# Kernel tuning notes

Measured on AMD Instinct MI355X. Metric: run time of the kernel, lower is better.

## Reference

```python
import jax, jax.numpy as jnp
import numpy as np

D = 1024
H = 16
HEAD_DIM = D // H

def setup_inputs() -> dict:
    key = jax.random.key(0)
    ks = jax.random.split(key, 5)
    B, T = 2, 2048
    scale = 0.02
    x = jax.random.normal(ks[0], (B, T, D), dtype=jnp.float32)
    W_kqv = jax.random.normal(ks[1], (D, 3 * D), dtype=jnp.float32) * scale
    b_kqv = jnp.zeros((3 * D,), dtype=jnp.float32)
    W_proj = jax.random.normal(ks[2], (D, D), dtype=jnp.float32) * scale
    b_proj = jnp.zeros((D,), dtype=jnp.float32)
    return {"x": x, "W_kqv": W_kqv, "b_kqv": b_kqv, "W_proj": W_proj, "b_proj": b_proj}

def reference(x, W_kqv, b_kqv, W_proj, b_proj):
    B, T, d = x.shape
    qkv = x @ W_kqv + b_kqv  # [B,T,3d]
    q, k, v = jnp.split(qkv, 3, axis=-1)
    # [B, h, T, head_dim]
    def heads(t):
        return t.reshape(B, T, H, HEAD_DIM).transpose(0, 2, 1, 3)
    q, k, v = heads(q), heads(k), heads(v)
    scores = jnp.einsum("bhqd,bhkd->bhqk", q, k) / jnp.sqrt(jnp.float32(HEAD_DIM))
    causal = jnp.tril(jnp.ones((T, T), dtype=bool))  # True = keep
    scores = jnp.where(causal[None, None], scores, -jnp.inf)
    attn = jax.nn.softmax(scores, axis=-1)
    out = jnp.einsum("bhqk,bhkd->bhqd", attn, v)
    out = out.transpose(0, 2, 1, 3).reshape(B, T, d)
    return out @ W_proj + b_proj
```

## Files before the change

kernel.cpp:

```cpp
#include <hip/hip_runtime.h>
#include <hip/hip_bf16.h>
#include <cstdint>

typedef __bf16 bf16_t;
typedef __bf16 bf16x8 __attribute__((ext_vector_type(8)));
typedef __bf16 bf16x4 __attribute__((ext_vector_type(4)));
typedef float  f32x4  __attribute__((ext_vector_type(4)));

static constexpr int Bb = 2;
static constexpr int Tt = 2048;
static constexpr int Dd = 1024;
static constexpr int Hh = 16;
static constexpr int HD = 64;

#define QSCALE 0.18033688011112042f

__device__ __forceinline__ void async_copy16(const bf16_t* gsrc, bf16_t* ldst) {
    __builtin_amdgcn_global_load_lds(
        (const __attribute__((address_space(1))) unsigned int*)gsrc,
        (__attribute__((address_space(3))) unsigned int*)ldst, 16, 0, 0);
}

__global__ __launch_bounds__(256) void prep_kernel(
    const float* __restrict__ x, bf16_t* __restrict__ x_bf,
    const float* __restrict__ Wk, bf16_t* __restrict__ wkqvt,
    const float* __restrict__ Wp, bf16_t* __restrict__ wprojt) {
    __shared__ bf16_t tile[64][72];
    int bid = blockIdx.x;
    int t = threadIdx.x;
    if (bid < 2048) {
        int i = (bid * 256 + t) * 8;
        float4 v0 = *(const float4*)(x + i);
        float4 v1 = *(const float4*)(x + i + 4);
        bf16x8 o;
        o[0] = (bf16_t)v0.x; o[1] = (bf16_t)v0.y; o[2] = (bf16_t)v0.z; o[3] = (bf16_t)v0.w;
        o[4] = (bf16_t)v1.x; o[5] = (bf16_t)v1.y; o[6] = (bf16_t)v1.z; o[7] = (bf16_t)v1.w;
        *(bf16x8*)(x_bf + i) = o;
        return;
    }
    const float* in; bf16_t* out; int R, C, tr, tc;
    if (bid < 2816) {
        int id = bid - 2048;
        R = Dd; C = 3 * Dd;
        tc = (id % 48) * 64; tr = (id / 48) * 64;
        in = Wk; out = wkqvt;
    } else {
        int id = bid - 2816;
        R = Dd; C = Dd;
        tc = (id & 15) * 64; tr = (id >> 4) * 64;
        in = Wp; out = wprojt;
    }
    int r = t >> 4;
    int c4 = (t & 15) * 4;
#pragma unroll
    for (int rr = 0; rr < 4; ++rr) {
        int row = r + rr * 16;
        float4 v = *(const float4*)(in + (size_t)(tr + row) * C + tc + c4);
        tile[c4 + 0][row] = (bf16_t)v.x;
        tile[c4 + 1][row] = (bf16_t)v.y;
        tile[c4 + 2][row] = (bf16_t)v.z;
        tile[c4 + 3][row] = (bf16_t)v.w;
    }
    __syncthreads();
#pragma unroll
    for (int rr = 0; rr < 4; ++rr) {
        int oc = r + rr * 16;
        bf16x4 o;
        o[0] = tile[oc][c4 + 0];
        o[1] = tile[oc][c4 + 1];
        o[2] = tile[oc][c4 + 2];
        o[3] = tile[oc][c4 + 3];
        *(bf16x4*)(out + (size_t)(tc + oc) * R + tr + c4) = o;
    }
}

template <int MODE, int NT>
__global__ __launch_bounds__(256) void gemm_bt(
    const bf16_t* __restrict__ A, const bf16_t* __restrict__ Bt,
    const float* __restrict__ bias, float* __restrict__ Cout,
    bf16_t* __restrict__ qb_, bf16_t* __restrict__ kb_, bf16_t* __restrict__ vb_,
    int M, int N, int K) {
    constexpr int NFRAG = NT / 32;
    __shared__ bf16_t As[128 * 64];
    __shared__ bf16_t Bs[NT * 64];
    int t = threadIdx.x;
    int wave = t >> 6, lane = t & 63;
    int l15 = lane & 15, quad = lane >> 4;
    int wm = wave & 1, wn = wave >> 1;
    int m0 = blockIdx.y * 128, n0 = blockIdx.x * NT;

    f32x4 acc[4][NFRAG];
#pragma unroll
    for (int mi = 0; mi < 4; ++mi)
#pragma unroll
        for (int ni = 0; ni < NFRAG; ++ni) acc[mi][ni] = (f32x4){0.f, 0.f, 0.f, 0.f};

    int kx = l15 & 7;

    for (int kk = 0; kk < K; kk += 64) {
        __syncthreads();
#pragma unroll
        for (int j = 0; j < 4; ++j) {
            int cid = j * 256 + t;
            int row = cid >> 3, sub = (cid & 7) ^ (row & 7);
            async_copy16(A + (size_t)(m0 + row) * K + kk + sub * 8, &As[cid * 8]);
        }
#pragma unroll
        for (int j = 0; j < NT / 32; ++j) {
            int cid = j * 256 + t;
            int row = cid >> 3, sub = (cid & 7) ^ (row & 7);
            async_copy16(Bt + (size_t)(n0 + row) * K + kk + sub * 8, &Bs[cid * 8]);
        }
        __syncthreads();
#pragma unroll
        for (int kb = 0; kb < 2; ++kb) {
            bf16x8 af[4], bf[NFRAG];
#pragma unroll
            for (int mi = 0; mi < 4; ++mi) {
                int r = wm * 64 + mi * 16 + l15;
                af[mi] = *(const bf16x8*)(&As[r * 64 + ((kb * 4 + quad) ^ kx) * 8]);
            }
#pragma unroll
            for (int ni = 0; ni < NFRAG; ++ni) {
                int r = wn * (NT / 2) + ni * 16 + l15;
                bf[ni] = *(const bf16x8*)(&Bs[r * 64 + ((kb * 4 + quad) ^ kx) * 8]);
            }
#pragma unroll
            for (int mi = 0; mi < 4; ++mi)
#pragma unroll
                for (int ni = 0; ni < NFRAG; ++ni)
                    acc[mi][ni] = __builtin_amdgcn_mfma_f32_16x16x32_bf16(af[mi], bf[ni], acc[mi][ni], 0, 0, 0);
        }
    }

    if (MODE == 1 && (n0 >> 10) == 2) {
#pragma unroll
        for (int ni = 0; ni < NFRAG; ++ni) {
            int col = n0 + wn * (NT / 2) + ni * 16 + l15;
            float bv = bias[col];
            int hh = (col >> 6) & 15, dd = col & 63;
#pragma unroll
            for (int mi = 0; mi < 4; ++mi) {
                int row = m0 + wm * 64 + mi * 16 + quad * 4;
                int bb = row >> 11, tt = row & (Tt - 1);
                bf16x4 pv;
#pragma unroll
                for (int r = 0; r < 4; ++r) pv[r] = (bf16_t)(acc[mi][ni][r] + bv);
                *(bf16x4*)(vb_ + ((size_t)(bb * Hh + hh) * HD + dd) * Tt + tt) = pv;
            }
        }
        return;
    }

#pragma unroll
    for (int ni = 0; ni < NFRAG; ++ni) {
        int col = n0 + wn * (NT / 2) + ni * 16 + l15;
        float bv = bias[col];
#pragma unroll
        for (int mi = 0; mi < 4; ++mi) {
#pragma unroll
            for (int r = 0; r < 4; ++r) {
                int row = m0 + wm * 64 + mi * 16 + quad * 4 + r;
                float v = acc[mi][ni][r] + bv;
                if (MODE == 0) {
                    Cout[(size_t)row * N + col] = v;
                } else {
                    int sec = col >> 10;
                    int hh = (col >> 6) & 15, dd = col & 63;
                    int bb = row >> 11, tt = row & (Tt - 1);
                    size_t idx = (((size_t)(bb * Hh + hh)) * Tt + tt) * HD + dd;
                    if (sec == 0) qb_[idx] = (bf16_t)(v * QSCALE);
                    else          kb_[idx] = (bf16_t)v;
                }
            }
        }
    }
}

__global__ __launch_bounds__(256, 4) void attn_kernel(
    const bf16_t* __restrict__ qb, const bf16_t* __restrict__ kb,
    const bf16_t* __restrict__ vb, bf16_t* __restrict__ ab) {
    __shared__ bf16_t Ks[64][72];
    __shared__ bf16_t Vs[64][72];
    __shared__ bf16_t Ps[4][16][72];
    int t = threadIdx.x;
    int wave = t >> 6, lane = t & 63;
    int l15 = lane & 15, quad = lane >> 4;
    int bh = blockIdx.x;
    int qt = 31 - (int)blockIdx.y;
    int b = bh >> 4, h = bh & 15;
    int qbase = qt * 64 + wave * 16;
    int q = qbase + l15;
    const bf16_t* qptr = qb + (size_t)bh * Tt * HD;
    const bf16_t* kptr = kb + (size_t)bh * Tt * HD;
    const bf16_t* vptr = vb + (size_t)bh * HD * Tt;

    bf16x8 qf[2];
    qf[0] = *(const bf16x8*)(qptr + (size_t)q * HD + quad * 8);
    qf[1] = *(const bf16x8*)(qptr + (size_t)q * HD + 32 + quad * 8);

    f32x4 o[4];
#pragma unroll
    for (int g = 0; g < 4; ++g) o[g] = (f32x4){0.f, 0.f, 0.f, 0.f};
    float mrow = -1e30f, lrow = 0.f;

    int srow = t >> 2;
    int scol = (t & 3) * 16;
    int qmax_w = qbase + 15;

    int nkt = qt + 1;
    for (int it = 0; it < nkt; ++it) {
        int kt0 = it * 64;
        __syncthreads();
        const bf16_t* kg = kptr + (size_t)(kt0 + srow) * HD + scol;
        *(bf16x8*)(&Ks[srow][scol])     = *(const bf16x8*)(kg);
        *(bf16x8*)(&Ks[srow][scol + 8]) = *(const bf16x8*)(kg + 8);
        const bf16_t* vg = vptr + (size_t)srow * Tt + kt0 + scol;
        *(bf16x8*)(&Vs[srow][scol])     = *(const bf16x8*)(vg);
        *(bf16x8*)(&Vs[srow][scol + 8]) = *(const bf16x8*)(vg + 8);
        __syncthreads();
        if (kt0 > qmax_w) continue;

        f32x4 s[4];
#pragma unroll
        for (int g = 0; g < 4; ++g) {
            s[g] = (f32x4){0.f, 0.f, 0.f, 0.f};
            bf16x8 kf0 = *(const bf16x8*)(&Ks[g * 16 + l15][quad * 8]);
            bf16x8 kf1 = *(const bf16x8*)(&Ks[g * 16 + l15][32 + quad * 8]);
            s[g] = __builtin_amdgcn_mfma_f32_16x16x32_bf16(kf0, qf[0], s[g], 0, 0, 0);
            s[g] = __builtin_amdgcn_mfma_f32_16x16x32_bf16(kf1, qf[1], s[g], 0, 0, 0);
        }

        if (kt0 + 63 > qbase) {
#pragma unroll
            for (int g = 0; g < 4; ++g)
#pragma unroll
                for (int r = 0; r < 4; ++r) {
                    int k_abs = kt0 + g * 16 + quad * 4 + r;
                    s[g][r] = (k_abs > q) ? -1e30f : s[g][r];
                }
        }

        float mloc = -1e30f;
#pragma unroll
        for (int g = 0; g < 4; ++g)
            mloc = fmaxf(mloc, fmaxf(fmaxf(s[g][0], s[g][1]), fmaxf(s[g][2], s[g][3])));
        mloc = fmaxf(mloc, __shfl_xor(mloc, 16));
        mloc = fmaxf(mloc, __shfl_xor(mloc, 32));
        float mnew = fmaxf(mrow, mloc);
        float alpha = exp2f(mrow - mnew);
        mrow = mnew;

        float rs = 0.f;
#pragma unroll
        for (int g = 0; g < 4; ++g) {
            float p0 = exp2f(s[g][0] - mnew);
            float p1 = exp2f(s[g][1] - mnew);
            float p2 = exp2f(s[g][2] - mnew);
            float p3 = exp2f(s[g][3] - mnew);
            rs += (p0 + p1) + (p2 + p3);
            bf16x4 pk;
            pk[0] = (bf16_t)p0; pk[1] = (bf16_t)p1; pk[2] = (bf16_t)p2; pk[3] = (bf16_t)p3;
            *(bf16x4*)(&Ps[wave][l15][g * 16 + quad * 4]) = pk;
        }
        rs += __shfl_xor(rs, 16);
        rs += __shfl_xor(rs, 32);
        lrow = lrow * alpha + rs;

#pragma unroll
        for (int g = 0; g < 4; ++g)
#pragma unroll
            for (int r = 0; r < 4; ++r) o[g][r] *= alpha;

#pragma unroll
        for (int kc = 0; kc < 2; ++kc) {
            bf16x8 pf = *(const bf16x8*)(&Ps[wave][l15][kc * 32 + quad * 8]);
#pragma unroll
            for (int g = 0; g < 4; ++g) {
                bf16x8 vf = *(const bf16x8*)(&Vs[g * 16 + l15][kc * 32 + quad * 8]);
                o[g] = __builtin_amdgcn_mfma_f32_16x16x32_bf16(vf, pf, o[g], 0, 0, 0);
            }
        }
    }

    float inv = 1.0f / lrow;
    size_t obase = ((size_t)b * Tt + q) * Dd + h * 64;
#pragma unroll
    for (int g = 0; g < 4; ++g) {
        bf16x4 ov;
#pragma unroll
        for (int r = 0; r < 4; ++r) ov[r] = (bf16_t)(o[g][r] * inv);
        *(bf16x4*)(ab + obase + g * 16 + quad * 4) = ov;
    }
}

extern "C" void kernel_launch(void* const* d_in, const int* in_sizes, int n_in,
                              void* d_out, int out_size, void* d_ws, size_t ws_size,
                              hipStream_t stream) {
    const float* x      = (const float*)d_in[0];
    const float* W_kqv  = (const float*)d_in[1];
    const float* b_kqv  = (const float*)d_in[2];
    const float* W_proj = (const float*)d_in[3];
    const float* b_proj = (const float*)d_in[4];
    float* out = (float*)d_out;
    char* ws = (char*)d_ws;
    const size_t MB = 1ull << 20;
    bf16_t* x_bf   = (bf16_t*)(ws + 0 * MB);
    bf16_t* wkqvt  = (bf16_t*)(ws + 8 * MB);
    bf16_t* wprojt = (bf16_t*)(ws + 14 * MB);
    bf16_t* qb     = (bf16_t*)(ws + 16 * MB);
    bf16_t* kb     = (bf16_t*)(ws + 24 * MB);
    bf16_t* vb     = (bf16_t*)(ws + 32 * MB);
    bf16_t* ab     = (bf16_t*)(ws + 40 * MB);

    prep_kernel<<<3072, 256, 0, stream>>>(x, x_bf, W_kqv, wkqvt, W_proj, wprojt);
    gemm_bt<1, 128><<<dim3(3 * Dd / 128, Bb * Tt / 128), 256, 0, stream>>>(
        x_bf, wkqvt, b_kqv, nullptr, qb, kb, vb, Bb * Tt, 3 * Dd, Dd);
    attn_kernel<<<dim3(Bb * Hh, 32), 256, 0, stream>>>(qb, kb, vb, ab);
    gemm_bt<0, 64><<<dim3(Dd / 64, Bb * Tt / 128), 256, 0, stream>>>(
        ab, wprojt, b_proj, out, nullptr, nullptr, nullptr, Bb * Tt, Dd, Dd);
}
```

Measured before the change: 194.2 us.

## Prefetch next K/V tile into registers and vectorize GEMM epilogue stores

The attention kernel now loads the next K/V tile from global memory into registers while the current tile is being computed, so global latency overlaps with MFMA work. The early-skip check for fully masked tiles is removed. Separately, the GEMM swaps the MFMA operand order so each lane holds four consecutive output columns. This allows float4 bias loads and vectorized f32x4/bf16x4 stores for the output, Q and K epilogues, at the cost of scattered scalar stores for the transposed V layout. Register pressure in the attention kernel rises from holding the prefetched tile.

```diff
diff --git a/kernel.cpp b/kernel.cpp
--- a/kernel.cpp
+++ b/kernel.cpp
@@ -129,50 +129,58 @@
             for (int mi = 0; mi < 4; ++mi)
 #pragma unroll
                 for (int ni = 0; ni < NFRAG; ++ni)
-                    acc[mi][ni] = __builtin_amdgcn_mfma_f32_16x16x32_bf16(af[mi], bf[ni], acc[mi][ni], 0, 0, 0);
-        }
-    }
-
-    if (MODE == 1 && (n0 >> 10) == 2) {
+                    acc[mi][ni] = __builtin_amdgcn_mfma_f32_16x16x32_bf16(bf[ni], af[mi], acc[mi][ni], 0, 0, 0);
+        }
+    }
+
+    int sec = n0 >> 10;
+    if (MODE == 1 && sec == 2) {
 #pragma unroll
         for (int ni = 0; ni < NFRAG; ++ni) {
-            int col = n0 + wn * (NT / 2) + ni * 16 + l15;
-            float bv = bias[col];
-            int hh = (col >> 6) & 15, dd = col & 63;
+            int n = n0 + wn * (NT / 2) + ni * 16 + quad * 4;
+            int hh = (n >> 6) & 15, dd0 = n & 63;
+            f32x4 bv4 = *(const f32x4*)(bias + n);
 #pragma unroll
             for (int mi = 0; mi < 4; ++mi) {
-                int row = m0 + wm * 64 + mi * 16 + quad * 4;
+                int row = m0 + wm * 64 + mi * 16 + l15;
+                int bb = row >> 11, tt = row & (Tt - 1);
+#pragma unroll
+                for (int r = 0; r < 4; ++r)
+                    vb_[((size_t)(bb * Hh + hh) * HD + dd0 + r) * Tt + tt] =
+                        (bf16_t)(acc[mi][ni][r] + bv4[r]);
+            }
+        }
+        return;
+    }
+    if (MODE == 1) {
+        float sc = (sec == 0) ? QSCALE : 1.0f;
+        bf16_t* dst = (sec == 0) ? qb_ : kb_;
+#pragma unroll
+        for (int ni = 0; ni < NFRAG; ++ni) {
+            int n = n0 + wn * (NT / 2) + ni * 16 + quad * 4;
+            int hh = (n >> 6) & 15, dd0 = n & 63;
+            f32x4 bv4 = *(const f32x4*)(bias + n);
+#pragma unroll
+            for (int mi = 0; mi < 4; ++mi) {
+                int row = m0 + wm * 64 + mi * 16 + l15;
                 int bb = row >> 11, tt = row & (Tt - 1);
                 bf16x4 pv;
 #pragma unroll
-                for (int r = 0; r < 4; ++r) pv[r] = (bf16_t)(acc[mi][ni][r] + bv);
-                *(bf16x4*)(vb_ + ((size_t)(bb * Hh + hh) * HD + dd) * Tt + tt) = pv;
+                for (int r = 0; r < 4; ++r) pv[r] = (bf16_t)((acc[mi][ni][r] + bv4[r]) * sc);
+                *(bf16x4*)(dst + ((size_t)(bb * Hh + hh) * Tt + tt) * HD + dd0) = pv;
             }
         }
         return;
     }
-
-#pragma unroll
-    for (int ni = 0; ni < NFRAG; ++ni) {
-        int col = n0 + wn * (NT / 2) + ni * 16 + l15;
-        float bv = bias[col];
-#pragma unroll
-        for (int mi = 0; mi < 4; ++mi) {
-#pragma unroll
-            for (int r = 0; r < 4; ++r) {
-                int row = m0 + wm * 64 + mi * 16 + quad * 4 + r;
-                float v = acc[mi][ni][r] + bv;
-                if (MODE == 0) {
-                    Cout[(size_t)row * N + col] = v;
-                } else {
-                    int sec = col >> 10;
-                    int hh = (col >> 6) & 15, dd = col & 63;
-                    int bb = row >> 11, tt = row & (Tt - 1);
-                    size_t idx = (((size_t)(bb * Hh + hh)) * Tt + tt) * HD + dd;
-                    if (sec == 0) qb_[idx] = (bf16_t)(v * QSCALE);
-                    else          kb_[idx] = (bf16_t)v;
-                }
-            }
+#pragma unroll
+    for (int mi = 0; mi < 4; ++mi) {
+        int m = m0 + wm * 64 + mi * 16 + l15;
+#pragma unroll
+        for (int ni = 0; ni < NFRAG; ++ni) {
+            int n = n0 + wn * (NT / 2) + ni * 16 + quad * 4;
+            f32x4 bv4 = *(const f32x4*)(bias + n);
+            f32x4 ov = acc[mi][ni] + bv4;
+            *(f32x4*)(Cout + (size_t)m * N + n) = ov;
         }
     }
 }
@@ -206,20 +214,36 @@
 
     int srow = t >> 2;
     int scol = (t & 3) * 16;
-    int qmax_w = qbase + 15;
 
     int nkt = qt + 1;
+
+    bf16x8 kr0, kr1, vr0, vr1;
+    {
+        const bf16_t* kg = kptr + (size_t)srow * HD + scol;
+        kr0 = *(const bf16x8*)(kg);
+        kr1 = *(const bf16x8*)(kg + 8);
+        const bf16_t* vg = vptr + (size_t)srow * Tt + scol;
+        vr0 = *(const bf16x8*)(vg);
+        vr1 = *(const bf16x8*)(vg + 8);
+    }
+
     for (int it = 0; it < nkt; ++it) {
         int kt0 = it * 64;
         __syncthreads();
-        const bf16_t* kg = kptr + (size_t)(kt0 + srow) * HD + scol;
-        *(bf16x8*)(&Ks[srow][scol])     = *(const bf16x8*)(kg);
-        *(bf16x8*)(&Ks[srow][scol + 8]) = *(const bf16x8*)(kg + 8);
-        const bf16_t* vg = vptr + (size_t)srow * Tt + kt0 + scol;
-        *(bf16x8*)(&Vs[srow][scol])     = *(const bf16x8*)(vg);
-        *(bf16x8*)(&Vs[srow][scol + 8]) = *(const bf16x8*)(vg + 8);
+        *(bf16x8*)(&Ks[srow][scol])     = kr0;
+        *(bf16x8*)(&Ks[srow][scol + 8]) = kr1;
+        *(bf16x8*)(&Vs[srow][scol])     = vr0;
+        *(bf16x8*)(&Vs[srow][scol + 8]) = vr1;
         __syncthreads();
-        if (kt0 > qmax_w) continue;
+        if (it + 1 < nkt) {
+            int kt = (it + 1) * 64;
+            const bf16_t* kg = kptr + (size_t)(kt + srow) * HD + scol;
+            kr0 = *(const bf16x8*)(kg);
+            kr1 = *(const bf16x8*)(kg + 8);
+            const bf16_t* vg = vptr + (size_t)srow * Tt + kt + scol;
+            vr0 = *(const bf16x8*)(vg);
+            vr1 = *(const bf16x8*)(vg + 8);
+        }
 
         f32x4 s[4];
 #pragma unroll
```

After: 191.8 us. No clear change (-1.2%).
